# Kernel optimization log

Measured on AMD Instinct MI355X. Metric: run time of the kernel, lower is better.

Reference implementation:

```python
import jax, jax.numpy as jnp
import numpy as np

N_NODES = 50000
N_EDGES = 800000
N_GRAPHS = 64


def setup_inputs() -> dict:
    key = jax.random.key(0)
    ks = jax.random.split(key, 16)
    x = jax.random.normal(ks[0], (N_NODES, 3), dtype=jnp.float32)
    edge_index = jax.random.randint(ks[1], (2, N_EDGES), 0, N_NODES, dtype=jnp.int32)
    batch = jnp.sort(jax.random.randint(ks[2], (N_NODES,), 0, N_GRAPHS, dtype=jnp.int32))
    def glorot(k, shape):
        fan_in, fan_out = shape
        lim = (6.0 / (fan_in + fan_out)) ** 0.5
        return jax.random.uniform(k, shape, jnp.float32, -lim, lim)
    return {
        "x": x,
        "edge_index": edge_index,
        "batch": batch,
        "W1": glorot(ks[3], (3, 64)),   "b1": jnp.zeros((64,), jnp.float32),
        "W2": glorot(ks[4], (64, 128)), "b2": jnp.zeros((128,), jnp.float32),
        "W3": glorot(ks[5], (128, 128)),"b3": jnp.zeros((128,), jnp.float32),
        "Wf1": glorot(ks[6], (128, 64)),"bf1": jnp.zeros((64,), jnp.float32),
        "Wf2": glorot(ks[7], (64, 10)), "bf2": jnp.zeros((10,), jnp.float32),
    }


def _gcn_conv(h, src, dst, norm, W, b, n_nodes):
    h = h @ W                                   # [N, out]
    msg = h[src] * norm[:, None]                # gather + scale  [E+N, out]
    agg = jax.ops.segment_sum(msg, dst, num_segments=n_nodes)  # scatter-add
    return agg + b


def reference(x, edge_index, batch, W1, b1, W2, b2, W3, b3, Wf1, bf1, Wf2, bf2):
    n = x.shape[0]
    loop = jnp.arange(n, dtype=edge_index.dtype)
    src = jnp.concatenate([edge_index[0], loop])  # add self-loops once
    dst = jnp.concatenate([edge_index[1], loop])
    deg = jax.ops.segment_sum(jnp.ones_like(dst, jnp.float32), dst, num_segments=n)
    dinv = jax.lax.rsqrt(deg)                     # deg >= 1 (self-loops)
    norm = dinv[src] * dinv[dst]

    h = jax.nn.relu(_gcn_conv(x, src, dst, norm, W1, b1, n))
    h = jax.nn.relu(_gcn_conv(h, src, dst, norm, W2, b2, n))
    h = jax.nn.relu(_gcn_conv(h, src, dst, norm, W3, b3, n))

    # global mean pool over graphs in the batch
    sums = jax.ops.segment_sum(h, batch, num_segments=N_GRAPHS)      # [G, 128]
    cnts = jax.ops.segment_sum(jnp.ones((n,), jnp.float32), batch, num_segments=N_GRAPHS)
    pooled = sums / jnp.maximum(cnts, 1.0)[:, None]

    h = jax.nn.relu(pooled @ Wf1 + bf1)
    return h @ Wf2 + bf2  # dropout is identity at inference
```

## Files before the change

### kernel.cpp

```cpp
#include <hip/hip_runtime.h>

#define N_NODES 50000
#define N_EDGES 800000
#define N_GRAPHS 64
#define SCAN_B 256
#define SCAN_NBLK ((N_NODES + SCAN_B - 1) / SCAN_B)
#define FILL_E 2048

typedef __attribute__((ext_vector_type(8))) short short8;
typedef __attribute__((ext_vector_type(4))) float floatx4;

__device__ __forceinline__ unsigned short f2bf(float f) {
    unsigned int u = __float_as_uint(f);
    u += 0x7FFFu + ((u >> 16) & 1u);
    return (unsigned short)(u >> 16);
}
__device__ __forceinline__ float bf2f(unsigned short h) {
    return __uint_as_float(((unsigned int)h) << 16);
}
__device__ __forceinline__ float blo(unsigned int u) { return __uint_as_float(u << 16); }
__device__ __forceinline__ float bhi(unsigned int u) { return __uint_as_float(u & 0xffff0000u); }


__global__ void k_prep(int* bcnt, float* pooled,
                       const float* __restrict__ W2, const float* __restrict__ W3,
                       unsigned short* Wb2, unsigned short* Wb3) {
    int i = blockIdx.x * blockDim.x + threadIdx.x;
    if (i < 256) bcnt[i] = 0;
    int j = i - 256;
    if (j >= 0 && j < N_GRAPHS * 128) pooled[j] = 0.0f;
    int k = i - 256 - N_GRAPHS * 128;
    if (k >= 0 && k < 64 * 128) {
        int kk = k >> 7, n = k & 127;
        Wb2[(((kk >> 3) * 128) + n) * 8 + (kk & 7)] = f2bf(W2[k]);
    }
    int l = i - 256 - N_GRAPHS * 128 - 64 * 128;
    if (l >= 0 && l < 128 * 128) {
        int kk = l >> 7, n = l & 127;
        Wb3[(((kk >> 3) * 128) + n) * 8 + (kk & 7)] = f2bf(W3[l]);
    }
}


__global__ __launch_bounds__(256) void k_bhist(const int* __restrict__ dst, int* bcnt) {
    __shared__ int bins[SCAN_NBLK];
    int t = threadIdx.x;
    for (int i = t; i < SCAN_NBLK; i += 256) bins[i] = 0;
    __syncthreads();
    int stride = gridDim.x * blockDim.x;
    for (int i4 = blockIdx.x * blockDim.x + t; i4 < N_EDGES / 4; i4 += stride) {
        int4 d = ((const int4*)dst)[i4];
        atomicAdd(&bins[d.x >> 8], 1);
        atomicAdd(&bins[d.y >> 8], 1);
        atomicAdd(&bins[d.z >> 8], 1);
        atomicAdd(&bins[d.w >> 8], 1);
    }
    __syncthreads();
    for (int i = t; i < SCAN_NBLK; i += 256)
        if (bins[i]) atomicAdd(&bcnt[i], bins[i]);
}

__global__ __launch_bounds__(256) void k_bscan(const int* __restrict__ bcnt,
                                               int* bstart, int* bcursor) {
    __shared__ int s[256];
    int t = threadIdx.x;
    int c = (t < SCAN_NBLK) ? bcnt[t] : 0;
    s[t] = c;
    __syncthreads();
    for (int off = 1; off < 256; off <<= 1) {
        int v = (t >= off) ? s[t - off] : 0;
        __syncthreads();
        s[t] += v;
        __syncthreads();
    }
    int excl = s[t] - c;
    bstart[t] = excl;
    bcursor[t] = excl;
    if (t == 255) bstart[256] = s[255];
}

__global__ __launch_bounds__(256) void k_binfill(const int* __restrict__ src,
                                                 const int* __restrict__ dst,
                                                 int* bcursor, int2* __restrict__ bpair) {
    __shared__ int cnt[SCAN_B];
    __shared__ int sc[SCAN_B];
    __shared__ int base[SCAN_B];
    __shared__ int delta[SCAN_B];
    __shared__ int ofs[SCAN_B];
    __shared__ int2 stage[FILL_E];
    __shared__ unsigned char bk[FILL_E];
    int tid = threadIdx.x;
    int e0 = blockIdx.x * FILL_E + tid * 8;
    cnt[tid] = 0; ofs[tid] = 0;
    __syncthreads();
    int s[8], d[8], bb[8];
    bool active = e0 < N_EDGES;
    if (active) {
        int4 sa = *(const int4*)(src + e0);
        int4 sb = *(const int4*)(src + e0 + 4);
        int4 da = *(const int4*)(dst + e0);
        int4 db = *(const int4*)(dst + e0 + 4);
        s[0]=sa.x; s[1]=sa.y; s[2]=sa.z; s[3]=sa.w;
        s[4]=sb.x; s[5]=sb.y; s[6]=sb.z; s[7]=sb.w;
        d[0]=da.x; d[1]=da.y; d[2]=da.z; d[3]=da.w;
        d[4]=db.x; d[5]=db.y; d[6]=db.z; d[7]=db.w;
#pragma unroll
        for (int k = 0; k < 8; ++k) {
            bb[k] = d[k] >> 8;
            atomicAdd(&cnt[bb[k]], 1);
        }
    }
    __syncthreads();
    int c = cnt[tid];
    sc[tid] = c;
    __syncthreads();
    for (int off = 1; off < SCAN_B; off <<= 1) {
        int v = (tid >= off) ? sc[tid - off] : 0;
        __syncthreads();
        sc[tid] += v;
        __syncthreads();
    }
    base[tid] = sc[tid] - c;
    if (c > 0) delta[tid] = atomicAdd(&bcursor[tid], c) - base[tid];
    __syncthreads();
    if (active) {
#pragma unroll
        for (int k = 0; k < 8; ++k) {
            int p = base[bb[k]] + atomicAdd(&ofs[bb[k]], 1);
            stage[p] = make_int2(s[k], d[k]);
            bk[p] = (unsigned char)bb[k];
        }
    }
    __syncthreads();
    int total = base[SCAN_B - 1] + cnt[SCAN_B - 1];
    for (int i = tid; i < total; i += 256)
        bpair[delta[bk[i]] + i] = stage[i];
}

__global__ __launch_bounds__(256) void k_build(const int2* __restrict__ bpair,
                                               const int* __restrict__ bstart,
                                               int* row_ptr, int* __restrict__ csr_src,
                                               float* dinv,
                                               const float* __restrict__ x,
                                               float* __restrict__ xs) {
    __shared__ int cnt[SCAN_B];
    __shared__ int sc[SCAN_B];
    __shared__ int cur[SCAN_B];
    int b = blockIdx.x, t = threadIdx.x;
    int start = bstart[b], end = bstart[b + 1];
    cnt[t] = 0;
    __syncthreads();
    for (int i = start + t; i < end; i += 256)
        atomicAdd(&cnt[bpair[i].y & (SCAN_B - 1)], 1);
    __syncthreads();
    int c = cnt[t];
    sc[t] = c;
    __syncthreads();
    for (int off = 1; off < SCAN_B; off <<= 1) {
        int v = (t >= off) ? sc[t - off] : 0;
        __syncthreads();
        sc[t] += v;
        __syncthreads();
    }
    int pos = start + sc[t] - c;
    cur[t] = pos;
    int n = b * SCAN_B + t;
    if (n < N_NODES) {
        row_ptr[n] = pos;
        float di = rsqrtf((float)(c + 1));
        dinv[n] = di;
        xs[n * 3 + 0] = x[n * 3 + 0] * di;
        xs[n * 3 + 1] = x[n * 3 + 1] * di;
        xs[n * 3 + 2] = x[n * 3 + 2] * di;
    }
    if (n == N_NODES) row_ptr[N_NODES] = N_EDGES;
    __syncthreads();
    for (int i = start + t; i < end; i += 256) {
        int2 pr = bpair[i];
        int p = atomicAdd(&cur[pr.y & (SCAN_B - 1)], 1);
        csr_src[p] = pr.x;
    }
}


__global__ void k_agg3(const float* __restrict__ xs, const int* __restrict__ row_ptr,
                       const int* __restrict__ csr_src, const float* __restrict__ dinv,
                       float* __restrict__ out) {
    int n = blockIdx.x * blockDim.x + threadIdx.x;
    if (n >= N_NODES) return;
    int lo = row_ptr[n], hi = row_ptr[n + 1];
    float a0 = xs[n * 3 + 0], a1 = xs[n * 3 + 1], a2 = xs[n * 3 + 2];
    for (int i = lo; i < hi; ++i) {
        int s = csr_src[i];
        a0 += xs[s * 3 + 0];
        a1 += xs[s * 3 + 1];
        a2 += xs[s * 3 + 2];
    }
    float din = dinv[n];
    out[n * 3 + 0] = a0 * din;
    out[n * 3 + 1] = a1 * din;
    out[n * 3 + 2] = a2 * din;
}

template<int IN_W, int OUT_W, int NPB>
__global__ void k_node_gemm(const float* __restrict__ h, const float* __restrict__ W,
                            const float* __restrict__ b, const float* __restrict__ dinv,
                            unsigned short* __restrict__ hb) {
    __shared__ float rows[NPB][IN_W];
    int n0 = blockIdx.x * NPB;
    int j = threadIdx.x;
    for (int t = j; t < NPB * IN_W; t += OUT_W) {
        int m = t / IN_W, k = t - m * IN_W;
        int n = n0 + m;
        rows[m][k] = (n < N_NODES) ? h[(size_t)n * IN_W + k] : 0.0f;
    }
    __syncthreads();
    float acc[NPB];
    float bj = b[j];
#pragma unroll
    for (int m = 0; m < NPB; ++m) acc[m] = bj;
#pragma unroll
    for (int k = 0; k < IN_W; ++k) {
        float wk = W[k * OUT_W + j];
#pragma unroll
        for (int m = 0; m < NPB; ++m) acc[m] += rows[m][k] * wk;
    }
#pragma unroll
    for (int m = 0; m < NPB; ++m) {
        int n = n0 + m;
        if (n < N_NODES)
            hb[(size_t)n * OUT_W + j] = f2bf(fmaxf(acc[m], 0.0f) * dinv[n]);
    }
}


__global__ void k_agg64(const unsigned short* __restrict__ hb, const int* __restrict__ row_ptr,
                        const int* __restrict__ csr_src, const float* __restrict__ dinv,
                        unsigned short* __restrict__ outb) {
    int wv = (blockIdx.x * blockDim.x + threadIdx.x) >> 6;
    int lane = threadIdx.x & 63;
    if (wv >= N_NODES) return;
    int q = lane & 7;
    int slot = lane >> 3;
    int lo = row_ptr[wv], hi = row_ptr[wv + 1];
    const uint4* hbv = (const uint4*)hb;
    float acc[8];
#pragma unroll
    for (int i = 0; i < 8; ++i) acc[i] = 0.f;
    if (slot == 0) {
        uint4 u = hbv[(size_t)wv * 8 + q];
        acc[0] += blo(u.x); acc[1] += bhi(u.x);
        acc[2] += blo(u.y); acc[3] += bhi(u.y);
        acc[4] += blo(u.z); acc[5] += bhi(u.z);
        acc[6] += blo(u.w); acc[7] += bhi(u.w);
    }
    for (int base = lo; base < hi; base += 32) {
#pragma unroll
        for (int k = 0; k < 4; ++k) {
            int e = base + k * 8 + slot;
            int ee = e < hi ? e : hi - 1;
            int s = csr_src[ee];
            uint4 u = hbv[(size_t)s * 8 + q];
            if (e < hi) {
                acc[0] += blo(u.x); acc[1] += bhi(u.x);
                acc[2] += blo(u.y); acc[3] += bhi(u.y);
                acc[4] += blo(u.z); acc[5] += bhi(u.z);
                acc[6] += blo(u.w); acc[7] += bhi(u.w);
            }
        }
    }
#pragma unroll
    for (int i = 0; i < 8; ++i) {
        acc[i] += __shfl_xor(acc[i], 8);
        acc[i] += __shfl_xor(acc[i], 16);
        acc[i] += __shfl_xor(acc[i], 32);
    }
    if (slot == 0) {
        float din = dinv[wv];
        uint4 w;
        w.x = (unsigned int)f2bf(acc[0] * din) | ((unsigned int)f2bf(acc[1] * din) << 16);
        w.y = (unsigned int)f2bf(acc[2] * din) | ((unsigned int)f2bf(acc[3] * din) << 16);
        w.z = (unsigned int)f2bf(acc[4] * din) | ((unsigned int)f2bf(acc[5] * din) << 16);
        w.w = (unsigned int)f2bf(acc[6] * din) | ((unsigned int)f2bf(acc[7] * din) << 16);
        ((uint4*)outb)[(size_t)wv * 8 + q] = w;
    }
}

__global__ void k_agg128(const unsigned short* __restrict__ hb, const int* __restrict__ row_ptr,
                         const int* __restrict__ csr_src, const float* __restrict__ dinv,
                         unsigned short* __restrict__ outb) {
    int wv = (blockIdx.x * blockDim.x + threadIdx.x) >> 6;
    int lane = threadIdx.x & 63;
    if (wv >= N_NODES) return;
    int q = lane & 15;
    int slot = lane >> 4;
    int lo = row_ptr[wv], hi = row_ptr[wv + 1];
    const uint4* hbv = (const uint4*)hb;
    float acc[8];
#pragma unroll
    for (int i = 0; i < 8; ++i) acc[i] = 0.f;
    if (slot == 0) {
        uint4 u = hbv[(size_t)wv * 16 + q];
        acc[0] += blo(u.x); acc[1] += bhi(u.x);
        acc[2] += blo(u.y); acc[3] += bhi(u.y);
        acc[4] += blo(u.z); acc[5] += bhi(u.z);
        acc[6] += blo(u.w); acc[7] += bhi(u.w);
    }
    for (int base = lo; base < hi; base += 16) {
#pragma unroll
        for (int k = 0; k < 4; ++k) {
            int e = base + k * 4 + slot;
            int ee = e < hi ? e : hi - 1;
            int s = csr_src[ee];
            uint4 u = hbv[(size_t)s * 16 + q];
            if (e < hi) {
                acc[0] += blo(u.x); acc[1] += bhi(u.x);
                acc[2] += blo(u.y); acc[3] += bhi(u.y);
                acc[4] += blo(u.z); acc[5] += bhi(u.z);
                acc[6] += blo(u.w); acc[7] += bhi(u.w);
            }
        }
    }
#pragma unroll
    for (int i = 0; i < 8; ++i) {
        acc[i] += __shfl_xor(acc[i], 16);
        acc[i] += __shfl_xor(acc[i], 32);
    }
    if (slot == 0) {
        float din = dinv[wv];
        uint4 w;
        w.x = (unsigned int)f2bf(acc[0] * din) | ((unsigned int)f2bf(acc[1] * din) << 16);
        w.y = (unsigned int)f2bf(acc[2] * din) | ((unsigned int)f2bf(acc[3] * din) << 16);
        w.z = (unsigned int)f2bf(acc[4] * din) | ((unsigned int)f2bf(acc[5] * din) << 16);
        w.w = (unsigned int)f2bf(acc[6] * din) | ((unsigned int)f2bf(acc[7] * din) << 16);
        ((uint4*)outb)[(size_t)wv * 16 + q] = w;
    }
}


__global__ __launch_bounds__(256) void k_gemm_l2_mfma(
    const unsigned short* __restrict__ Ab,
    const unsigned short* __restrict__ Wb,
    const float* __restrict__ b,
    const float* __restrict__ dinv,
    unsigned short* __restrict__ hb) {
    __shared__ float sC[64][128];
    int tid = threadIdx.x;
    int wave = tid >> 6, lane = tid & 63;
    int quad = lane >> 4, l16 = lane & 15;
    int n0 = blockIdx.x * 64;
    int arow = n0 + wave * 16 + l16;
    if (arow >= N_NODES) arow = N_NODES - 1;

    floatx4 acc[8];
#pragma unroll
    for (int t = 0; t < 8; ++t) acc[t] = (floatx4){0.f, 0.f, 0.f, 0.f};

#pragma unroll
    for (int ks = 0; ks < 2; ++ks) {
        short8 a = *(const short8*)(Ab + (size_t)arow * 64 + ks * 32 + quad * 8);
#pragma unroll
        for (int t = 0; t < 8; ++t) {
            short8 bf = *(const short8*)(Wb + (((ks * 4 + quad) * 128) + t * 16 + l16) * 8);
            acc[t] = __builtin_amdgcn_mfma_f32_16x16x32_bf16(a, bf, acc[t], 0, 0, 0);
        }
    }
#pragma unroll
    for (int t = 0; t < 8; ++t)
#pragma unroll
        for (int r = 0; r < 4; ++r)
            sC[wave * 16 + quad * 4 + r][t * 16 + l16] = acc[t][r];
    __syncthreads();
    int tn = tid >> 5, tj = tid & 31;
    float4 bv = *(const float4*)(b + tj * 4);
#pragma unroll
    for (int m = 0; m < 8; ++m) {
        int n = n0 + tn * 8 + m;
        if (n < N_NODES) {
            float di = dinv[n];
            unsigned short h0 = f2bf(fmaxf(sC[tn * 8 + m][tj * 4 + 0] + bv.x, 0.f) * di);
            unsigned short h1 = f2bf(fmaxf(sC[tn * 8 + m][tj * 4 + 1] + bv.y, 0.f) * di);
            unsigned short h2 = f2bf(fmaxf(sC[tn * 8 + m][tj * 4 + 2] + bv.z, 0.f) * di);
            unsigned short h3 = f2bf(fmaxf(sC[tn * 8 + m][tj * 4 + 3] + bv.w, 0.f) * di);
            uint2 w2;
            w2.x = (unsigned int)h0 | ((unsigned int)h1 << 16);
            w2.y = (unsigned int)h2 | ((unsigned int)h3 << 16);
            *(uint2*)(hb + (size_t)n * 128 + tj * 4) = w2;
        }
    }
}


__global__ __launch_bounds__(256) void k_gemm_l3_mfma_pool(
    const unsigned short* __restrict__ Ab,
    const unsigned short* __restrict__ Wb,
    const float* __restrict__ b,
    const int* __restrict__ batch,
    float* __restrict__ pooled) {
    __shared__ float sC[64][128];
    __shared__ float red[8][128];
    __shared__ int sb[64];
    int tid = threadIdx.x;
    int wave = tid >> 6, lane = tid & 63;
    int quad = lane >> 4, l16 = lane & 15;
    int n0 = blockIdx.x * 64;
    int arow = n0 + wave * 16 + l16;
    if (arow >= N_NODES) arow = N_NODES - 1;

    floatx4 acc[8];
#pragma unroll
    for (int t = 0; t < 8; ++t) acc[t] = (floatx4){0.f, 0.f, 0.f, 0.f};

#pragma unroll
    for (int ks = 0; ks < 4; ++ks) {
        short8 a = *(const short8*)(Ab + (size_t)arow * 128 + ks * 32 + quad * 8);
#pragma unroll
        for (int t = 0; t < 8; ++t) {
            short8 bf = *(const short8*)(Wb + (((ks * 4 + quad) * 128) + t * 16 + l16) * 8);
            acc[t] = __builtin_amdgcn_mfma_f32_16x16x32_bf16(a, bf, acc[t], 0, 0, 0);
        }
    }
#pragma unroll
    for (int t = 0; t < 8; ++t) {
        float bc = b[t * 16 + l16];
#pragma unroll
        for (int r = 0; r < 4; ++r)
            sC[wave * 16 + quad * 4 + r][t * 16 + l16] = fmaxf(acc[t][r] + bc, 0.f);
    }
    if (tid < 64) {
        int n = n0 + tid;
        sb[tid] = (n < N_NODES) ? batch[n] : -1;
    }
    __syncthreads();
    int g0 = sb[0];
    int last = (n0 + 63 < N_NODES) ? (n0 + 63) : (N_NODES - 1);
    int g1 = batch[last];
    int tn = tid >> 5, tj = tid & 31;
    for (int g = g0; g <= g1; ++g) {
        float p0 = 0.f, p1 = 0.f, p2 = 0.f, p3 = 0.f;
#pragma unroll
        for (int m = 0; m < 8; ++m) {
            if (sb[tn * 8 + m] == g) {
                p0 += sC[tn * 8 + m][tj * 4 + 0];
                p1 += sC[tn * 8 + m][tj * 4 + 1];
                p2 += sC[tn * 8 + m][tj * 4 + 2];
                p3 += sC[tn * 8 + m][tj * 4 + 3];
            }
        }
        red[tn][tj * 4 + 0] = p0;
        red[tn][tj * 4 + 1] = p1;
        red[tn][tj * 4 + 2] = p2;
        red[tn][tj * 4 + 3] = p3;
        __syncthreads();
        if (tid < 128) {
            float s = 0.f;
#pragma unroll
            for (int r = 0; r < 8; ++r) s += red[r][tid];
            atomicAdd(&pooled[g * 128 + tid], s);
        }
        __syncthreads();
    }
}


__device__ __forceinline__ int lower_bound_batch(const int* __restrict__ batch, int val) {
    int lo = 0, hi = N_NODES;
    while (lo < hi) {
        int mid = (lo + hi) >> 1;
        if (batch[mid] < val) lo = mid + 1; else hi = mid;
    }
    return lo;
}

__global__ void k_fc(const float* __restrict__ pooled, const int* __restrict__ batch,
                     const float* __restrict__ Wf1, const float* __restrict__ bf1,
                     const float* __restrict__ Wf2, const float* __restrict__ bf2,
                     float* __restrict__ out) {
    __shared__ float sp[128];
    __shared__ float sh1[64];
    int g = blockIdx.x;
    int t = threadIdx.x;
    int lo = lower_bound_batch(batch, g);
    int hi = lower_bound_batch(batch, g + 1);
    float inv = 1.0f / fmaxf((float)(hi - lo), 1.0f);
    sp[t] = pooled[g * 128 + t] * inv;
    __syncthreads();
    if (t < 64) {
        float acc = bf1[t];
#pragma unroll 8
        for (int k = 0; k < 128; ++k) acc += sp[k] * Wf1[k * 64 + t];
        sh1[t] = fmaxf(acc, 0.0f);
    }
    __syncthreads();
    if (t < 10) {
        float acc = bf2[t];
#pragma unroll 8
        for (int k = 0; k < 64; ++k) acc += sh1[k] * Wf2[k * 10 + t];
        out[g * 10 + t] = acc;
    }
}

extern "C" void kernel_launch(void* const* d_in, const int* in_sizes, int n_in,
                              void* d_out, int out_size, void* d_ws, size_t ws_size,
                              hipStream_t stream) {
    const float* x     = (const float*)d_in[0];
    const int*   ei    = (const int*)d_in[1];
    const int*   batch = (const int*)d_in[2];
    const float* W1  = (const float*)d_in[3];
    const float* b1  = (const float*)d_in[4];
    const float* W2  = (const float*)d_in[5];
    const float* b2  = (const float*)d_in[6];
    const float* W3  = (const float*)d_in[7];
    const float* b3  = (const float*)d_in[8];
    const float* Wf1 = (const float*)d_in[9];
    const float* bf1 = (const float*)d_in[10];
    const float* Wf2 = (const float*)d_in[11];
    const float* bf2 = (const float*)d_in[12];
    float* out = (float*)d_out;

    const int* src = ei;
    const int* dst = ei + N_EDGES;

    float* dinv   = (float*)d_ws;
    int*   bcnt   = (int*)(dinv + N_NODES);
    int*   bstart = bcnt + 256;
    int*   bcursor= bstart + 257;
    int*   row_ptr= bcursor + 256;
    int*   csr_src= row_ptr + N_NODES + 1;
    size_t o1 = (size_t)(csr_src + N_EDGES) - (size_t)d_ws;
    o1 = (o1 + 7) & ~(size_t)7;
    int2*  bpair  = (int2*)((char*)d_ws + o1);
    float* xs     = (float*)(bpair + N_EDGES);
    float* a3     = xs + (size_t)N_NODES * 3;
    unsigned short* Wb2 = (unsigned short*)(a3 + (size_t)N_NODES * 3);
    unsigned short* Wb3 = Wb2 + 64 * 128;
    size_t ofs = (size_t)(Wb3 + 128 * 128) - (size_t)d_ws;
    ofs = (ofs + 15) & ~(size_t)15;
    unsigned short* bufA = (unsigned short*)((char*)d_ws + ofs);
    unsigned short* hb   = bufA + (size_t)N_NODES * 128;
    float* pooled = (float*)(hb + (size_t)N_NODES * 128);

    const int TB = 256;
    const int GEMM_BLKS = (N_NODES + 63) / 64;
    const int PREP_N = 256 + N_GRAPHS * 128 + 64 * 128 + 128 * 128;
    const int BIN_BLKS = (N_EDGES + FILL_E - 1) / FILL_E;

    k_prep<<<(PREP_N + TB - 1) / TB, TB, 0, stream>>>(bcnt, pooled, W2, W3, Wb2, Wb3);
    k_bhist<<<256, 256, 0, stream>>>(dst, bcnt);
    k_bscan<<<1, 256, 0, stream>>>(bcnt, bstart, bcursor);
    k_binfill<<<BIN_BLKS, 256, 0, stream>>>(src, dst, bcursor, bpair);
    k_build<<<SCAN_NBLK, 256, 0, stream>>>(bpair, bstart, row_ptr, csr_src, dinv, x, xs);

    k_agg3<<<(N_NODES + TB - 1) / TB, TB, 0, stream>>>(xs, row_ptr, csr_src, dinv, a3);
    k_node_gemm<3, 64, 4><<<(N_NODES + 3) / 4, 64, 0, stream>>>(a3, W1, b1, dinv, hb);

    k_agg64<<<(N_NODES * 64 + TB - 1) / TB, TB, 0, stream>>>(hb, row_ptr, csr_src, dinv, bufA);
    k_gemm_l2_mfma<<<GEMM_BLKS, 256, 0, stream>>>(bufA, Wb2, b2, dinv, hb);

    k_agg128<<<(N_NODES * 64 + TB - 1) / TB, TB, 0, stream>>>(hb, row_ptr, csr_src, dinv, bufA);
    k_gemm_l3_mfma_pool<<<GEMM_BLKS, 256, 0, stream>>>(bufA, Wb3, b3, batch, pooled);

    k_fc<<<N_GRAPHS, 128, 0, stream>>>(pooled, batch, Wf1, bf1, Wf2, bf2, out);
}
```

Baseline: 238.5 us.

## Fuse prep into histogram, drop global atomics, fuse layer-1 aggregate with GEMM

Merges the weight-conversion and zeroing prep kernel into the histogram kernel. Each block now writes its private bin counts to a per-block array, which the scan kernel reduces, so no global atomics or bcnt zeroing are needed. Layer-1 aggregation and the 3x64 linear transform are fused into one kernel that writes bf16 rows directly, removing the a3 intermediate and a launch. In exchange, the single-block scan now does 256 strided reads per bin, and each thread in the fused kernel computes all 64 outputs serially.

```diff
diff --git a/kernel.cpp b/kernel.cpp
--- a/kernel.cpp
+++ b/kernel.cpp
@@ -22,33 +22,30 @@
 __device__ __forceinline__ float bhi(unsigned int u) { return __uint_as_float(u & 0xffff0000u); }
 
 
-__global__ void k_prep(int* bcnt, float* pooled,
-                       const float* __restrict__ W2, const float* __restrict__ W3,
-                       unsigned short* Wb2, unsigned short* Wb3) {
-    int i = blockIdx.x * blockDim.x + threadIdx.x;
-    if (i < 256) bcnt[i] = 0;
-    int j = i - 256;
-    if (j >= 0 && j < N_GRAPHS * 128) pooled[j] = 0.0f;
-    int k = i - 256 - N_GRAPHS * 128;
+__global__ __launch_bounds__(256) void k_hist_prep(const int* __restrict__ dst,
+                                                   int* __restrict__ bins_global,
+                                                   float* pooled,
+                                                   const float* __restrict__ W2,
+                                                   const float* __restrict__ W3,
+                                                   unsigned short* Wb2, unsigned short* Wb3) {
+    __shared__ int bins[SCAN_NBLK];
+    int t = threadIdx.x;
+    for (int i = t; i < SCAN_NBLK; i += 256) bins[i] = 0;
+    __syncthreads();
+    int gid = blockIdx.x * 256 + t;
+    if (gid < N_GRAPHS * 128) pooled[gid] = 0.0f;
+    int k = gid - N_GRAPHS * 128;
     if (k >= 0 && k < 64 * 128) {
         int kk = k >> 7, n = k & 127;
         Wb2[(((kk >> 3) * 128) + n) * 8 + (kk & 7)] = f2bf(W2[k]);
     }
-    int l = i - 256 - N_GRAPHS * 128 - 64 * 128;
+    int l = gid - N_GRAPHS * 128 - 64 * 128;
     if (l >= 0 && l < 128 * 128) {
         int kk = l >> 7, n = l & 127;
         Wb3[(((kk >> 3) * 128) + n) * 8 + (kk & 7)] = f2bf(W3[l]);
     }
-}
-
-
-__global__ __launch_bounds__(256) void k_bhist(const int* __restrict__ dst, int* bcnt) {
-    __shared__ int bins[SCAN_NBLK];
-    int t = threadIdx.x;
-    for (int i = t; i < SCAN_NBLK; i += 256) bins[i] = 0;
-    __syncthreads();
-    int stride = gridDim.x * blockDim.x;
-    for (int i4 = blockIdx.x * blockDim.x + t; i4 < N_EDGES / 4; i4 += stride) {
+    const int stride = 256 * 256;
+    for (int i4 = gid; i4 < N_EDGES / 4; i4 += stride) {
         int4 d = ((const int4*)dst)[i4];
         atomicAdd(&bins[d.x >> 8], 1);
         atomicAdd(&bins[d.y >> 8], 1);
@@ -57,14 +54,16 @@
     }
     __syncthreads();
     for (int i = t; i < SCAN_NBLK; i += 256)
-        if (bins[i]) atomicAdd(&bcnt[i], bins[i]);
-}
-
-__global__ __launch_bounds__(256) void k_bscan(const int* __restrict__ bcnt,
+        bins_global[blockIdx.x * SCAN_NBLK + i] = bins[i];
+}
+
+__global__ __launch_bounds__(256) void k_bscan(const int* __restrict__ bins_global,
                                                int* bstart, int* bcursor) {
     __shared__ int s[256];
     int t = threadIdx.x;
-    int c = (t < SCAN_NBLK) ? bcnt[t] : 0;
+    int c = 0;
+    if (t < SCAN_NBLK)
+        for (int r = 0; r < 256; ++r) c += bins_global[r * SCAN_NBLK + t];
     s[t] = c;
     __syncthreads();
     for (int off = 1; off < 256; off <<= 1) {
@@ -183,10 +182,18 @@
 }
 
 
-__global__ void k_agg3(const float* __restrict__ xs, const int* __restrict__ row_ptr,
-                       const int* __restrict__ csr_src, const float* __restrict__ dinv,
-                       float* __restrict__ out) {
-    int n = blockIdx.x * blockDim.x + threadIdx.x;
+__global__ __launch_bounds__(256) void k_l1_fused(
+    const float* __restrict__ xs, const int* __restrict__ row_ptr,
+    const int* __restrict__ csr_src, const float* __restrict__ dinv,
+    const float* __restrict__ W1, const float* __restrict__ b1,
+    unsigned short* __restrict__ hb) {
+    __shared__ float sW[192];
+    __shared__ float sb[64];
+    int t = threadIdx.x;
+    if (t < 192) sW[t] = W1[t];
+    if (t < 64) sb[t] = b1[t];
+    __syncthreads();
+    int n = blockIdx.x * 256 + t;
     if (n >= N_NODES) return;
     int lo = row_ptr[n], hi = row_ptr[n + 1];
     float a0 = xs[n * 3 + 0], a1 = xs[n * 3 + 1], a2 = xs[n * 3 + 2];
@@ -197,39 +204,21 @@
         a2 += xs[s * 3 + 2];
     }
     float din = dinv[n];
-    out[n * 3 + 0] = a0 * din;
-    out[n * 3 + 1] = a1 * din;
-    out[n * 3 + 2] = a2 * din;
-}
-
-template<int IN_W, int OUT_W, int NPB>
-__global__ void k_node_gemm(const float* __restrict__ h, const float* __restrict__ W,
-                            const float* __restrict__ b, const float* __restrict__ dinv,
-                            unsigned short* __restrict__ hb) {
-    __shared__ float rows[NPB][IN_W];
-    int n0 = blockIdx.x * NPB;
-    int j = threadIdx.x;
-    for (int t = j; t < NPB * IN_W; t += OUT_W) {
-        int m = t / IN_W, k = t - m * IN_W;
-        int n = n0 + m;
-        rows[m][k] = (n < N_NODES) ? h[(size_t)n * IN_W + k] : 0.0f;
-    }
-    __syncthreads();
-    float acc[NPB];
-    float bj = b[j];
-#pragma unroll
-    for (int m = 0; m < NPB; ++m) acc[m] = bj;
-#pragma unroll
-    for (int k = 0; k < IN_W; ++k) {
-        float wk = W[k * OUT_W + j];
-#pragma unroll
-        for (int m = 0; m < NPB; ++m) acc[m] += rows[m][k] * wk;
-    }
-#pragma unroll
-    for (int m = 0; m < NPB; ++m) {
-        int n = n0 + m;
-        if (n < N_NODES)
-            hb[(size_t)n * OUT_W + j] = f2bf(fmaxf(acc[m], 0.0f) * dinv[n]);
+    a0 *= din; a1 *= din; a2 *= din;
+    uint4* row = (uint4*)(hb + (size_t)n * 64);
+#pragma unroll
+    for (int j0 = 0; j0 < 64; j0 += 8) {
+        unsigned int h[4];
+#pragma unroll
+        for (int k = 0; k < 4; ++k) {
+            int j = j0 + 2 * k;
+            float v0 = a0 * sW[j] + a1 * sW[64 + j] + a2 * sW[128 + j] + sb[j];
+            float v1 = a0 * sW[j + 1] + a1 * sW[64 + j + 1] + a2 * sW[128 + j + 1] + sb[j + 1];
+            h[k] = (unsigned int)f2bf(fmaxf(v0, 0.f) * din)
+                 | ((unsigned int)f2bf(fmaxf(v1, 0.f) * din) << 16);
+        }
+        uint4 w; w.x = h[0]; w.y = h[1]; w.z = h[2]; w.w = h[3];
+        row[j0 >> 3] = w;
     }
 }
 
@@ -521,18 +510,17 @@
     const int* src = ei;
     const int* dst = ei + N_EDGES;
 
-    float* dinv   = (float*)d_ws;
-    int*   bcnt   = (int*)(dinv + N_NODES);
-    int*   bstart = bcnt + 256;
-    int*   bcursor= bstart + 257;
-    int*   row_ptr= bcursor + 256;
-    int*   csr_src= row_ptr + N_NODES + 1;
+    float* dinv      = (float*)d_ws;
+    int* bins_global = (int*)(dinv + N_NODES);
+    int* bstart      = bins_global + 256 * SCAN_NBLK;
+    int* bcursor     = bstart + 257;
+    int* row_ptr     = bcursor + 256;
+    int* csr_src     = row_ptr + N_NODES + 1;
     size_t o1 = (size_t)(csr_src + N_EDGES) - (size_t)d_ws;
     o1 = (o1 + 7) & ~(size_t)7;
-    int2*  bpair  = (int2*)((char*)d_ws + o1);
-    float* xs     = (float*)(bpair + N_EDGES);
-    float* a3     = xs + (size_t)N_NODES * 3;
-    unsigned short* Wb2 = (unsigned short*)(a3 + (size_t)N_NODES * 3);
+    int2* bpair      = (int2*)((char*)d_ws + o1);
+    float* xs        = (float*)(bpair + N_EDGES);
+    unsigned short* Wb2 = (unsigned short*)(xs + (size_t)N_NODES * 3);
     unsigned short* Wb3 = Wb2 + 64 * 128;
     size_t ofs = (size_t)(Wb3 + 128 * 128) - (size_t)d_ws;
     ofs = (ofs + 15) & ~(size_t)15;
@@ -542,17 +530,14 @@
 
     const int TB = 256;
     const int GEMM_BLKS = (N_NODES + 63) / 64;
-    const int PREP_N = 256 + N_GRAPHS * 128 + 64 * 128 + 128 * 128;
     const int BIN_BLKS = (N_EDGES + FILL_E - 1) / FILL_E;
 
-    k_prep<<<(PREP_N + TB - 1) / TB, TB, 0, stream>>>(bcnt, pooled, W2, W3, Wb2, Wb3);
-    k_bhist<<<256, 256, 0, stream>>>(dst, bcnt);
-    k_bscan<<<1, 256, 0, stream>>>(bcnt, bstart, bcursor);
+    k_hist_prep<<<256, 256, 0, stream>>>(dst, bins_global, pooled, W2, W3, Wb2, Wb3);
+    k_bscan<<<1, 256, 0, stream>>>(bins_global, bstart, bcursor);
     k_binfill<<<BIN_BLKS, 256, 0, stream>>>(src, dst, bcursor, bpair);
     k_build<<<SCAN_NBLK, 256, 0, stream>>>(bpair, bstart, row_ptr, csr_src, dinv, x, xs);
 
-    k_agg3<<<(N_NODES + TB - 1) / TB, TB, 0, stream>>>(xs, row_ptr, csr_src, dinv, a3);
-    k_node_gemm<3, 64, 4><<<(N_NODES + 3) / 4, 64, 0, stream>>>(a3, W1, b1, dinv, hb);
+    k_l1_fused<<<SCAN_NBLK, 256, 0, stream>>>(xs, row_ptr, csr_src, dinv, W1, b1, hb);
 
     k_agg64<<<(N_NODES * 64 + TB - 1) / TB, TB, 0, stream>>>(hb, row_ptr, csr_src, dinv, bufA);
     k_gemm_l2_mfma<<<GEMM_BLKS, 256, 0, stream>>>(bufA, Wb2, b2, dinv, hb);
```

Result: no change. 237.7 us (-0.3%).
